# Kernel optimization log

Measured on AMD Instinct MI355X. Metric: run time of the kernel, lower is better.

Reference implementation:

```python
import jax, jax.numpy as jnp
import numpy as np

B, H, W, Z = 4, 256, 256, 64
ITERATIONS = 8
EPSILON = 1e-06
CENTER = 6.0  # 7-point Laplacian diagonal


def _stencil(x):
    # x: [B, H, W, Z]; zero (Dirichlet) boundaries via padded shifts
    west = jnp.pad(x[:, :, :-1, :], ((0, 0), (0, 0), (1, 0), (0, 0)))
    east = jnp.pad(x[:, :, 1:, :], ((0, 0), (0, 0), (0, 1), (0, 0)))
    north = jnp.pad(x[:, :-1, :, :], ((0, 0), (1, 0), (0, 0), (0, 0)))
    south = jnp.pad(x[:, 1:, :, :], ((0, 0), (0, 1), (0, 0), (0, 0)))
    bottom = jnp.pad(x[:, :, :, :-1], ((0, 0), (0, 0), (0, 0), (1, 0)))
    top = jnp.pad(x[:, :, :, 1:], ((0, 0), (0, 0), (0, 0), (0, 1)))
    return CENTER * x - west - east - south - north - bottom - top


def _dot(a, b):
    # per-sample dot product, keepdims for scalar broadcast
    return jnp.sum(a * b, axis=(1, 2, 3), keepdims=True)


def setup_inputs() -> dict:
    key = jax.random.key(0)
    k1, k2, k3 = jax.random.split(key, 3)
    shape = (B, H, W, Z)
    return {
        "x": jax.random.normal(k1, shape, dtype=jnp.float32),
        "b": jax.random.normal(k2, shape, dtype=jnp.float32),
        "reference_sol": jax.random.normal(k3, shape, dtype=jnp.float32),
    }


def reference(x, b, reference_sol):
    r = b - _stencil(x)
    p = r
    rho = _dot(r, r)

    def body(carry, _):
        x, r, p, rho = carry
        w = _stencil(p)
        eta = _dot(p, w)
        alpha = rho / (eta + EPSILON)
        x = x + alpha * p
        r = r - alpha * w
        rho_next = _dot(r, r)
        beta = rho_next / (rho + EPSILON)
        p = r + beta * p
        return (x, r, p, rho_next), None

    (x, r, p, rho), _ = jax.lax.scan(body, (x, r, p, rho), None, length=ITERATIONS)

    diff = x - reference_sol
    loss = jnp.mean(diff * diff)
    max_error = jnp.max(jnp.abs(diff))
    residual_norm_sq = jnp.mean(rho)
    return (loss, x, max_error, residual_norm_sq)
```

## Files before the change

### kernel.cpp

```cpp
#include <hip/hip_runtime.h>

#define B_ 4
#define H_ 256
#define W_ 256
#define Z_ 64
#define NB_ (H_*W_*Z_)
#define N_  (B_*NB_)
#define ITER_ 8
#define EPS_ 1e-6f
#define SLOTS_ 64

#define RHO_OFF   0
#define ETA_OFF   ((ITER_+1)*B_*SLOTS_)
#define LOSS_OFF  (ETA_OFF + ITER_*B_*SLOTS_)
#define MAXE_OFF  (LOSS_OFF + SLOTS_)
#define SCAL_FLOATS (MAXE_OFF + SLOTS_)

struct F8 { float4 a, b; };

__device__ __forceinline__ float wsum(float v){
  v += __shfl_xor(v,32); v += __shfl_xor(v,16); v += __shfl_xor(v,8);
  v += __shfl_xor(v,4);  v += __shfl_xor(v,2);  v += __shfl_xor(v,1);
  return v;
}
__device__ __forceinline__ float wmaxr(float v){
  v = fmaxf(v,__shfl_xor(v,32)); v = fmaxf(v,__shfl_xor(v,16));
  v = fmaxf(v,__shfl_xor(v,8));  v = fmaxf(v,__shfl_xor(v,4));
  v = fmaxf(v,__shfl_xor(v,2));  v = fmaxf(v,__shfl_xor(v,1));
  return v;
}
__device__ __forceinline__ float read_sum(const float* s){
  return wsum(s[threadIdx.x & 63]);
}
__device__ __forceinline__ void block_atomic_sum(float v, float* dst, float* lds){
  v = wsum(v);
  int wid = threadIdx.x >> 6, lane = threadIdx.x & 63;
  if (lane == 0) lds[wid] = v;
  __syncthreads();
  if (threadIdx.x == 0) atomicAdd(dst, lds[0]+lds[1]+lds[2]+lds[3]);
}

__device__ __forceinline__ float4 ld4(const float* p){ return *(const float4*)p; }

__device__ __forceinline__ void sten_core(const F8& c, const F8& wm, const F8& wp,
                                          const F8& hm, const F8& hp,
                                          float zl, float zr, F8& st)
{
  st.a.x = 6.f*c.a.x - wm.a.x - wp.a.x - hm.a.x - hp.a.x - zl     - c.a.y;
  st.a.y = 6.f*c.a.y - wm.a.y - wp.a.y - hm.a.y - hp.a.y - c.a.x  - c.a.z;
  st.a.z = 6.f*c.a.z - wm.a.z - wp.a.z - hm.a.z - hp.a.z - c.a.y  - c.a.w;
  st.a.w = 6.f*c.a.w - wm.a.w - wp.a.w - hm.a.w - hp.a.w - c.a.z  - c.b.x;
  st.b.x = 6.f*c.b.x - wm.b.x - wp.b.x - hm.b.x - hp.b.x - c.a.w  - c.b.y;
  st.b.y = 6.f*c.b.y - wm.b.y - wp.b.y - hm.b.y - hp.b.y - c.b.x  - c.b.z;
  st.b.z = 6.f*c.b.z - wm.b.z - wp.b.z - hm.b.z - hp.b.z - c.b.y  - c.b.w;
  st.b.w = 6.f*c.b.w - wm.b.w - wp.b.w - hm.b.w - hp.b.w - c.b.z  - zr;
}

__device__ __forceinline__ void stencil1(const float* __restrict__ a, int base,
                                         int w, int h, int zc, F8& c, F8& st)
{
  c.a = ld4(a+base); c.b = ld4(a+base+4);
  F8 zero; zero.a = make_float4(0,0,0,0); zero.b = zero.a;
  F8 wm = zero, wp = zero, hm = zero, hp = zero;
  if (w > 0)    { wm.a = ld4(a+base-Z_);    wm.b = ld4(a+base-Z_+4); }
  if (w < W_-1) { wp.a = ld4(a+base+Z_);    wp.b = ld4(a+base+Z_+4); }
  if (h > 0)    { hm.a = ld4(a+base-W_*Z_); hm.b = ld4(a+base-W_*Z_+4); }
  if (h < H_-1) { hp.a = ld4(a+base+W_*Z_); hp.b = ld4(a+base+W_*Z_+4); }
  float zl = (zc > 0) ? a[base-1] : 0.f;
  float zr = (zc < 7) ? a[base+8] : 0.f;
  sten_core(c, wm, wp, hm, hp, zl, zr, st);
}

__device__ __forceinline__ F8 comb8(const float* r, const float* p, float beta, int idx){
  F8 o;
  float4 ra = ld4(r+idx), rb = ld4(r+idx+4);
  float4 pa = ld4(p+idx), pb = ld4(p+idx+4);
  o.a.x = ra.x + beta*pa.x; o.a.y = ra.y + beta*pa.y;
  o.a.z = ra.z + beta*pa.z; o.a.w = ra.w + beta*pa.w;
  o.b.x = rb.x + beta*pb.x; o.b.y = rb.y + beta*pb.y;
  o.b.z = rb.z + beta*pb.z; o.b.w = rb.w + beta*pb.w;
  return o;
}
__device__ __forceinline__ void stencil2(const float* __restrict__ r,
                                         const float* __restrict__ p, float beta,
                                         int base, int w, int h, int zc,
                                         F8& c, F8& st)
{
  c = comb8(r,p,beta,base);
  F8 zero; zero.a = make_float4(0,0,0,0); zero.b = zero.a;
  F8 wm = zero, wp = zero, hm = zero, hp = zero;
  if (w > 0)    wm = comb8(r,p,beta,base-Z_);
  if (w < W_-1) wp = comb8(r,p,beta,base+Z_);
  if (h > 0)    hm = comb8(r,p,beta,base-W_*Z_);
  if (h < H_-1) hp = comb8(r,p,beta,base+W_*Z_);
  float zl = (zc > 0) ? r[base-1] + beta*p[base-1] : 0.f;
  float zr = (zc < 7) ? r[base+8] + beta*p[base+8] : 0.f;
  sten_core(c, wm, wp, hm, hp, zl, zr, st);
}

#define IDX_SETUP \
  const int zc = threadIdx.x & 7; \
  const int wl = threadIdx.x >> 3; \
  const int w  = blockIdx.x*32 + wl; \
  const int h  = blockIdx.y; \
  const int bb = blockIdx.z; \
  const int base = ((bb*H_ + h)*W_ + w)*Z_ + zc*8; \
  const int flat = (blockIdx.z*gridDim.y + blockIdx.y)*gridDim.x + blockIdx.x; \
  const int slot = flat & (SLOTS_-1);

__global__ __launch_bounds__(256) void k_init(const float* __restrict__ x,
                                              const float* __restrict__ b,
                                              float* __restrict__ r,
                                              float* scal)
{
  __shared__ float lds[4];
  IDX_SETUP
  F8 c, st;
  stencil1(x, base, w, h, zc, c, st);
  float4 b0 = ld4(b+base), b1 = ld4(b+base+4);
  F8 rv;
  rv.a = make_float4(b0.x-st.a.x, b0.y-st.a.y, b0.z-st.a.z, b0.w-st.a.w);
  rv.b = make_float4(b1.x-st.b.x, b1.y-st.b.y, b1.z-st.b.z, b1.w-st.b.w);
  *(float4*)(r+base)   = rv.a;
  *(float4*)(r+base+4) = rv.b;
  float rho = rv.a.x*rv.a.x + rv.a.y*rv.a.y + rv.a.z*rv.a.z + rv.a.w*rv.a.w
            + rv.b.x*rv.b.x + rv.b.y*rv.b.y + rv.b.z*rv.b.z + rv.b.w*rv.b.w;
  block_atomic_sum(rho, scal + RHO_OFF + (0*B_+bb)*SLOTS_ + slot, lds);
}

__global__ __launch_bounds__(256) void k_a0(const float* __restrict__ r,
                                            float* __restrict__ pnew,
                                            float* scal)
{
  __shared__ float lds[4];
  IDX_SETUP
  F8 c, st;
  stencil1(r, base, w, h, zc, c, st);
  *(float4*)(pnew+base)   = c.a;
  *(float4*)(pnew+base+4) = c.b;
  float eta = c.a.x*st.a.x + c.a.y*st.a.y + c.a.z*st.a.z + c.a.w*st.a.w
            + c.b.x*st.b.x + c.b.y*st.b.y + c.b.z*st.b.z + c.b.w*st.b.w;
  block_atomic_sum(eta, scal + ETA_OFF + (0*B_+bb)*SLOTS_ + slot, lds);
}

__global__ __launch_bounds__(256) void k_a(const float* __restrict__ r,
                                           const float* __restrict__ pold,
                                           float* __restrict__ pnew,
                                           float* scal, int it)
{
  __shared__ float lds[4];
  IDX_SETUP
  float num = read_sum(scal + RHO_OFF + (it*B_+bb)*SLOTS_);
  float den = read_sum(scal + RHO_OFF + ((it-1)*B_+bb)*SLOTS_);
  float beta = num / (den + EPS_);
  F8 c, st;
  stencil2(r, pold, beta, base, w, h, zc, c, st);
  *(float4*)(pnew+base)   = c.a;
  *(float4*)(pnew+base+4) = c.b;
  float eta = c.a.x*st.a.x + c.a.y*st.a.y + c.a.z*st.a.z + c.a.w*st.a.w
            + c.b.x*st.b.x + c.b.y*st.b.y + c.b.z*st.b.z + c.b.w*st.b.w;
  block_atomic_sum(eta, scal + ETA_OFF + (it*B_+bb)*SLOTS_ + slot, lds);
}

__global__ __launch_bounds__(256) void k_b(float* __restrict__ x,
                                           float* __restrict__ r,
                                           const float* __restrict__ p,
                                           float* scal, int it)
{
  __shared__ float lds[4];
  IDX_SETUP
  float num = read_sum(scal + RHO_OFF + (it*B_+bb)*SLOTS_);
  float den = read_sum(scal + ETA_OFF + (it*B_+bb)*SLOTS_);
  float alpha = num / (den + EPS_);
  F8 c, st;
  stencil1(p, base, w, h, zc, c, st);
  float4 x0 = ld4(x+base), x1 = ld4(x+base+4);
  x0.x += alpha*c.a.x; x0.y += alpha*c.a.y; x0.z += alpha*c.a.z; x0.w += alpha*c.a.w;
  x1.x += alpha*c.b.x; x1.y += alpha*c.b.y; x1.z += alpha*c.b.z; x1.w += alpha*c.b.w;
  *(float4*)(x+base)   = x0;
  *(float4*)(x+base+4) = x1;
  float4 r0 = ld4(r+base), r1 = ld4(r+base+4);
  r0.x -= alpha*st.a.x; r0.y -= alpha*st.a.y; r0.z -= alpha*st.a.z; r0.w -= alpha*st.a.w;
  r1.x -= alpha*st.b.x; r1.y -= alpha*st.b.y; r1.z -= alpha*st.b.z; r1.w -= alpha*st.b.w;
  *(float4*)(r+base)   = r0;
  *(float4*)(r+base+4) = r1;
  float rho = r0.x*r0.x + r0.y*r0.y + r0.z*r0.z + r0.w*r0.w
            + r1.x*r1.x + r1.y*r1.y + r1.z*r1.z + r1.w*r1.w;
  block_atomic_sum(rho, scal + RHO_OFF + ((it+1)*B_+bb)*SLOTS_ + slot, lds);
}

__global__ __launch_bounds__(256) void k_b_fin(const float* __restrict__ x,
                                               const float* __restrict__ r,
                                               const float* __restrict__ p,
                                               const float* __restrict__ ref,
                                               float* __restrict__ out,
                                               float* scal, int it)
{
  __shared__ float xs[2048];
  __shared__ float lds[12];
  IDX_SETUP
  float num = read_sum(scal + RHO_OFF + (it*B_+bb)*SLOTS_);
  float den = read_sum(scal + ETA_OFF + (it*B_+bb)*SLOTS_);
  float alpha = num / (den + EPS_);
  F8 c, st;
  stencil1(p, base, w, h, zc, c, st);
  float4 x0 = ld4(x+base), x1 = ld4(x+base+4);
  x0.x += alpha*c.a.x; x0.y += alpha*c.a.y; x0.z += alpha*c.a.z; x0.w += alpha*c.a.w;
  x1.x += alpha*c.b.x; x1.y += alpha*c.b.y; x1.z += alpha*c.b.z; x1.w += alpha*c.b.w;
  float4 r0 = ld4(r+base), r1 = ld4(r+base+4);
  r0.x -= alpha*st.a.x; r0.y -= alpha*st.a.y; r0.z -= alpha*st.a.z; r0.w -= alpha*st.a.w;
  r1.x -= alpha*st.b.x; r1.y -= alpha*st.b.y; r1.z -= alpha*st.b.z; r1.w -= alpha*st.b.w;
  float rho = r0.x*r0.x + r0.y*r0.y + r0.z*r0.z + r0.w*r0.w
            + r1.x*r1.x + r1.y*r1.y + r1.z*r1.z + r1.w*r1.w;

  const int t = threadIdx.x;
  xs[t*8+0] = x0.x; xs[t*8+1] = x0.y; xs[t*8+2] = x0.z; xs[t*8+3] = x0.w;
  xs[t*8+4] = x1.x; xs[t*8+5] = x1.y; xs[t*8+6] = x1.z; xs[t*8+7] = x1.w;

  float4 f0 = ld4(ref+base), f1 = ld4(ref+base+4);
  float d0 = x0.x-f0.x, d1 = x0.y-f0.y, d2 = x0.z-f0.z, d3 = x0.w-f0.w;
  float d4 = x1.x-f1.x, d5 = x1.y-f1.y, d6 = x1.z-f1.z, d7 = x1.w-f1.w;
  float loss = d0*d0+d1*d1+d2*d2+d3*d3+d4*d4+d5*d5+d6*d6+d7*d7;
  float me = fmaxf(fmaxf(fmaxf(fabsf(d0),fabsf(d1)),fmaxf(fabsf(d2),fabsf(d3))),
                   fmaxf(fmaxf(fabsf(d4),fabsf(d5)),fmaxf(fabsf(d6),fabsf(d7))));

  float rs = wsum(rho), ls = wsum(loss), ms = wmaxr(me);
  int wid = t >> 6, lane = t & 63;
  if (lane == 0) { lds[wid] = rs; lds[4+wid] = ls; lds[8+wid] = ms; }
  __syncthreads();
  if (t == 0) {
    atomicAdd(scal + RHO_OFF + ((it+1)*B_+bb)*SLOTS_ + slot, lds[0]+lds[1]+lds[2]+lds[3]);
    atomicAdd(scal + LOSS_OFF + slot, lds[4]+lds[5]+lds[6]+lds[7]);
    float bm = fmaxf(fmaxf(lds[8],lds[9]), fmaxf(lds[10],lds[11]));
    atomicMax((unsigned int*)(scal + MAXE_OFF) + slot, __float_as_uint(bm));
  }

  const int S = flat * 2048;
  #pragma unroll
  for (int c2 = 0; c2 < 2; ++c2) {
    int q = t + 256*c2;
    if (q < 511) {
      float4 v = make_float4(xs[3+4*q], xs[4+4*q], xs[5+4*q], xs[6+4*q]);
      *(float4*)(out + S + 4 + 4*q) = v;
    } else if (q == 511) {
      out[S+1] = xs[0]; out[S+2] = xs[1]; out[S+3] = xs[2];
      out[S+2048] = xs[2047];
    }
  }
}

__global__ __launch_bounds__(64) void k_scal(const float* scal, float* out)
{
  int lane = threadIdx.x;
  float loss = wsum(scal[LOSS_OFF + lane]);
  float me   = wmaxr(__uint_as_float(((const unsigned int*)scal)[MAXE_OFF + lane]));
  float rho_sum = 0.f;
  for (int bb = 0; bb < B_; ++bb)
    rho_sum += wsum(scal[RHO_OFF + (ITER_*B_+bb)*SLOTS_ + lane]);
  if (lane == 0) {
    out[0]      = loss / (float)N_;
    out[1+N_]   = me;
    out[2+N_]   = rho_sum / (float)B_;
  }
}

extern "C" void kernel_launch(void* const* d_in, const int* in_sizes, int n_in,
                              void* d_out, int out_size, void* d_ws, size_t ws_size,
                              hipStream_t stream) {
  float* x         = (float*)d_in[0];
  const float* b   = (const float*)d_in[1];
  const float* ref = (const float*)d_in[2];
  float* out       = (float*)d_out;

  float* r  = (float*)d_ws;
  float* p0 = r + N_;
  float* p1;
  float* scal;
  size_t need3 = ((size_t)3*N_ + SCAL_FLOATS) * sizeof(float);
  if (ws_size >= need3) {
    p1   = p0 + N_;
    scal = p1 + N_;
  } else {
    p1   = (float*)d_out;
    scal = p0 + N_;
  }

  (void)hipMemsetAsync(scal, 0, SCAL_FLOATS*sizeof(float), stream);

  dim3 grid(W_/32, H_, B_), blk(256);
  k_init<<<grid, blk, 0, stream>>>(x, b, r, scal);

  float* pa = p1;
  float* pb = p0;
  for (int it = 0; it < ITER_; ++it) {
    if (it == 0)
      k_a0<<<grid, blk, 0, stream>>>(r, pa, scal);
    else
      k_a<<<grid, blk, 0, stream>>>(r, pb, pa, scal, it);
    if (it < ITER_-1)
      k_b<<<grid, blk, 0, stream>>>(x, r, pa, scal, it);
    else
      k_b_fin<<<grid, blk, 0, stream>>>(x, r, pa, ref, out, scal, it);
    float* t = pa; pa = pb; pb = t;
  }

  k_scal<<<1, 64, 0, stream>>>(scal, out);
}
```

Measured before the change: 1.097 ms.

## Fuse all CG phases into one persistent kernel with a software grid barrier

Replaces the 17 separate kernel launches with a single persistent kernel of 2048 blocks. Each block walks four tiles per phase, and the phases are separated by a hand-written atomic grid barrier built from 64 counters plus a generation flag. It also fetches the z-neighbour halo with wavefront shuffles instead of extra global loads, and pads the LDS staging buffer used in the final x write. This is meant to remove launch gaps and kernel tail effects, but it depends on all 2048 blocks being resident at once (launch bounds 256x8) or the barrier deadlocks, and each barrier adds spin-wait latency.

New measurement: 3.344 ms. +204.8%, slower.

```diff
diff --git a/kernel.cpp b/kernel.cpp
--- a/kernel.cpp
+++ b/kernel.cpp
@@ -10,11 +10,19 @@
 #define EPS_ 1e-6f
 #define SLOTS_ 64
 
+#define GRID_  2048
+#define TPB_   256
+#define NTILE_ 8192
+#define TILES_ (NTILE_/GRID_)
+static_assert(NTILE_ % GRID_ == 0, "tile split");
+
 #define RHO_OFF   0
 #define ETA_OFF   ((ITER_+1)*B_*SLOTS_)
 #define LOSS_OFF  (ETA_OFF + ITER_*B_*SLOTS_)
 #define MAXE_OFF  (LOSS_OFF + SLOTS_)
-#define SCAL_FLOATS (MAXE_OFF + SLOTS_)
+#define BAR_OFF   (MAXE_OFF + SLOTS_)
+#define GEN_OFF   (BAR_OFF + 64)
+#define SCAL_FLOATS (GEN_OFF + 32)
 
 struct F8 { float4 a, b; };
 
@@ -38,37 +46,42 @@
   if (lane == 0) lds[wid] = v;
   __syncthreads();
   if (threadIdx.x == 0) atomicAdd(dst, lds[0]+lds[1]+lds[2]+lds[3]);
+  __syncthreads();
 }
 
 __device__ __forceinline__ float4 ld4(const float* p){ return *(const float4*)p; }
 
-__device__ __forceinline__ void sten_core(const F8& c, const F8& wm, const F8& wp,
-                                          const F8& hm, const F8& hp,
-                                          float zl, float zr, F8& st)
-{
-  st.a.x = 6.f*c.a.x - wm.a.x - wp.a.x - hm.a.x - hp.a.x - zl     - c.a.y;
-  st.a.y = 6.f*c.a.y - wm.a.y - wp.a.y - hm.a.y - hp.a.y - c.a.x  - c.a.z;
-  st.a.z = 6.f*c.a.z - wm.a.z - wp.a.z - hm.a.z - hp.a.z - c.a.y  - c.a.w;
-  st.a.w = 6.f*c.a.w - wm.a.w - wp.a.w - hm.a.w - hp.a.w - c.a.z  - c.b.x;
-  st.b.x = 6.f*c.b.x - wm.b.x - wp.b.x - hm.b.x - hp.b.x - c.a.w  - c.b.y;
-  st.b.y = 6.f*c.b.y - wm.b.y - wp.b.y - hm.b.y - hp.b.y - c.b.x  - c.b.z;
-  st.b.z = 6.f*c.b.z - wm.b.z - wp.b.z - hm.b.z - hp.b.z - c.b.y  - c.b.w;
-  st.b.w = 6.f*c.b.w - wm.b.w - wp.b.w - hm.b.w - hp.b.w - c.b.z  - zr;
+__device__ __forceinline__ void sub8(F8& s, const F8& n){
+  s.a.x-=n.a.x; s.a.y-=n.a.y; s.a.z-=n.a.z; s.a.w-=n.a.w;
+  s.b.x-=n.b.x; s.b.y-=n.b.y; s.b.z-=n.b.z; s.b.w-=n.b.w;
+}
+
+__device__ __forceinline__ void zcore(const F8& c, int zc, F8& st){
+  const int lane = threadIdx.x & 63;
+  float zl = __shfl(c.b.w, (lane-1)&63);
+  float zr = __shfl(c.a.x, (lane+1)&63);
+  zl = (zc > 0) ? zl : 0.f;
+  zr = (zc < 7) ? zr : 0.f;
+  st.a.x = 6.f*c.a.x - zl    - c.a.y;
+  st.a.y = 6.f*c.a.y - c.a.x - c.a.z;
+  st.a.z = 6.f*c.a.z - c.a.y - c.a.w;
+  st.a.w = 6.f*c.a.w - c.a.z - c.b.x;
+  st.b.x = 6.f*c.b.x - c.a.w - c.b.y;
+  st.b.y = 6.f*c.b.y - c.b.x - c.b.z;
+  st.b.z = 6.f*c.b.z - c.b.y - c.b.w;
+  st.b.w = 6.f*c.b.w - c.b.z - zr;
 }
 
 __device__ __forceinline__ void stencil1(const float* __restrict__ a, int base,
                                          int w, int h, int zc, F8& c, F8& st)
 {
   c.a = ld4(a+base); c.b = ld4(a+base+4);
-  F8 zero; zero.a = make_float4(0,0,0,0); zero.b = zero.a;
-  F8 wm = zero, wp = zero, hm = zero, hp = zero;
-  if (w > 0)    { wm.a = ld4(a+base-Z_);    wm.b = ld4(a+base-Z_+4); }
-  if (w < W_-1) { wp.a = ld4(a+base+Z_);    wp.b = ld4(a+base+Z_+4); }
-  if (h > 0)    { hm.a = ld4(a+base-W_*Z_); hm.b = ld4(a+base-W_*Z_+4); }
-  if (h < H_-1) { hp.a = ld4(a+base+W_*Z_); hp.b = ld4(a+base+W_*Z_+4); }
-  float zl = (zc > 0) ? a[base-1] : 0.f;
-  float zr = (zc < 7) ? a[base+8] : 0.f;
-  sten_core(c, wm, wp, hm, hp, zl, zr, st);
+  zcore(c, zc, st);
+  F8 t;
+  if (w > 0)    { t.a = ld4(a+base-Z_);    t.b = ld4(a+base-Z_+4);    sub8(st,t); }
+  if (w < W_-1) { t.a = ld4(a+base+Z_);    t.b = ld4(a+base+Z_+4);    sub8(st,t); }
+  if (h > 0)    { t.a = ld4(a+base-W_*Z_); t.b = ld4(a+base-W_*Z_+4); sub8(st,t); }
+  if (h < H_-1) { t.a = ld4(a+base+W_*Z_); t.b = ld4(a+base+W_*Z_+4); sub8(st,t); }
 }
 
 __device__ __forceinline__ F8 comb8(const float* r, const float* p, float beta, int idx){
@@ -87,180 +100,220 @@
                                          F8& c, F8& st)
 {
   c = comb8(r,p,beta,base);
-  F8 zero; zero.a = make_float4(0,0,0,0); zero.b = zero.a;
-  F8 wm = zero, wp = zero, hm = zero, hp = zero;
-  if (w > 0)    wm = comb8(r,p,beta,base-Z_);
-  if (w < W_-1) wp = comb8(r,p,beta,base+Z_);
-  if (h > 0)    hm = comb8(r,p,beta,base-W_*Z_);
-  if (h < H_-1) hp = comb8(r,p,beta,base+W_*Z_);
-  float zl = (zc > 0) ? r[base-1] + beta*p[base-1] : 0.f;
-  float zr = (zc < 7) ? r[base+8] + beta*p[base+8] : 0.f;
-  sten_core(c, wm, wp, hm, hp, zl, zr, st);
-}
-
-#define IDX_SETUP \
-  const int zc = threadIdx.x & 7; \
-  const int wl = threadIdx.x >> 3; \
-  const int w  = blockIdx.x*32 + wl; \
-  const int h  = blockIdx.y; \
-  const int bb = blockIdx.z; \
-  const int base = ((bb*H_ + h)*W_ + w)*Z_ + zc*8; \
-  const int flat = (blockIdx.z*gridDim.y + blockIdx.y)*gridDim.x + blockIdx.x; \
-  const int slot = flat & (SLOTS_-1);
-
-__global__ __launch_bounds__(256) void k_init(const float* __restrict__ x,
-                                              const float* __restrict__ b,
-                                              float* __restrict__ r,
-                                              float* scal)
+  zcore(c, zc, st);
+  if (w > 0)    sub8(st, comb8(r,p,beta,base-Z_));
+  if (w < W_-1) sub8(st, comb8(r,p,beta,base+Z_));
+  if (h > 0)    sub8(st, comb8(r,p,beta,base-W_*Z_));
+  if (h < H_-1) sub8(st, comb8(r,p,beta,base+W_*Z_));
+}
+
+__device__ __forceinline__ void gsync(unsigned* bars, unsigned* gen, unsigned epoch){
+  __syncthreads();
+  if (threadIdx.x == 0) {
+    __threadfence();
+    __hip_atomic_fetch_add(&bars[blockIdx.x & 63], 1u,
+                           __ATOMIC_RELAXED, __HIP_MEMORY_SCOPE_AGENT);
+  }
+  if (blockIdx.x == 0) {
+    if (threadIdx.x < 64) {
+      const unsigned tgt = epoch * (GRID_/64);
+      while (__hip_atomic_load(&bars[threadIdx.x],
+                               __ATOMIC_RELAXED, __HIP_MEMORY_SCOPE_AGENT) < tgt)
+        __builtin_amdgcn_s_sleep(2);
+    }
+    __syncthreads();
+    if (threadIdx.x == 0) {
+      __threadfence();
+      __hip_atomic_fetch_add(gen, 1u, __ATOMIC_RELAXED, __HIP_MEMORY_SCOPE_AGENT);
+    }
+  } else {
+    if (threadIdx.x == 0) {
+      while (__hip_atomic_load(gen, __ATOMIC_RELAXED,
+                               __HIP_MEMORY_SCOPE_AGENT) < epoch)
+        __builtin_amdgcn_s_sleep(2);
+      __threadfence();
+    }
+  }
+  __syncthreads();
+}
+
+#define TILE_OF(j) ((((int)(blockIdx.x >> 3) * TILES_ + (j)) << 3) | (int)(blockIdx.x & 7))
+
+#define TILE_SETUP(T) \
+  const int tx = (T) & 7; \
+  const int hh = ((T) >> 3) & 255; \
+  const int bb = (T) >> 11; \
+  const int w  = tx*32 + wl; \
+  const int base = ((bb*H_ + hh)*W_ + w)*Z_ + zc*8; \
+  const int slot = (T) & 63;
+
+#define XI(k) ((((k) >> 3)*9) + ((k) & 7))
+
+__global__ __launch_bounds__(TPB_, 8)
+void k_cg(float* x, const float* __restrict__ bv, const float* __restrict__ ref,
+          float* out, float* __restrict__ r, float* p0, float* p1,
+          float* __restrict__ scal)
 {
-  __shared__ float lds[4];
-  IDX_SETUP
-  F8 c, st;
-  stencil1(x, base, w, h, zc, c, st);
-  float4 b0 = ld4(b+base), b1 = ld4(b+base+4);
-  F8 rv;
-  rv.a = make_float4(b0.x-st.a.x, b0.y-st.a.y, b0.z-st.a.z, b0.w-st.a.w);
-  rv.b = make_float4(b1.x-st.b.x, b1.y-st.b.y, b1.z-st.b.z, b1.w-st.b.w);
-  *(float4*)(r+base)   = rv.a;
-  *(float4*)(r+base+4) = rv.b;
-  float rho = rv.a.x*rv.a.x + rv.a.y*rv.a.y + rv.a.z*rv.a.z + rv.a.w*rv.a.w
-            + rv.b.x*rv.b.x + rv.b.y*rv.b.y + rv.b.z*rv.b.z + rv.b.w*rv.b.w;
-  block_atomic_sum(rho, scal + RHO_OFF + (0*B_+bb)*SLOTS_ + slot, lds);
-}
-
-__global__ __launch_bounds__(256) void k_a0(const float* __restrict__ r,
-                                            float* __restrict__ pnew,
-                                            float* scal)
-{
-  __shared__ float lds[4];
-  IDX_SETUP
-  F8 c, st;
-  stencil1(r, base, w, h, zc, c, st);
-  *(float4*)(pnew+base)   = c.a;
-  *(float4*)(pnew+base+4) = c.b;
-  float eta = c.a.x*st.a.x + c.a.y*st.a.y + c.a.z*st.a.z + c.a.w*st.a.w
-            + c.b.x*st.b.x + c.b.y*st.b.y + c.b.z*st.b.z + c.b.w*st.b.w;
-  block_atomic_sum(eta, scal + ETA_OFF + (0*B_+bb)*SLOTS_ + slot, lds);
-}
-
-__global__ __launch_bounds__(256) void k_a(const float* __restrict__ r,
-                                           const float* __restrict__ pold,
-                                           float* __restrict__ pnew,
-                                           float* scal, int it)
-{
-  __shared__ float lds[4];
-  IDX_SETUP
-  float num = read_sum(scal + RHO_OFF + (it*B_+bb)*SLOTS_);
-  float den = read_sum(scal + RHO_OFF + ((it-1)*B_+bb)*SLOTS_);
-  float beta = num / (den + EPS_);
-  F8 c, st;
-  stencil2(r, pold, beta, base, w, h, zc, c, st);
-  *(float4*)(pnew+base)   = c.a;
-  *(float4*)(pnew+base+4) = c.b;
-  float eta = c.a.x*st.a.x + c.a.y*st.a.y + c.a.z*st.a.z + c.a.w*st.a.w
-            + c.b.x*st.b.x + c.b.y*st.b.y + c.b.z*st.b.z + c.b.w*st.b.w;
-  block_atomic_sum(eta, scal + ETA_OFF + (it*B_+bb)*SLOTS_ + slot, lds);
-}
-
-__global__ __launch_bounds__(256) void k_b(float* __restrict__ x,
-                                           float* __restrict__ r,
-                                           const float* __restrict__ p,
-                                           float* scal, int it)
-{
-  __shared__ float lds[4];
-  IDX_SETUP
-  float num = read_sum(scal + RHO_OFF + (it*B_+bb)*SLOTS_);
-  float den = read_sum(scal + ETA_OFF + (it*B_+bb)*SLOTS_);
-  float alpha = num / (den + EPS_);
-  F8 c, st;
-  stencil1(p, base, w, h, zc, c, st);
-  float4 x0 = ld4(x+base), x1 = ld4(x+base+4);
-  x0.x += alpha*c.a.x; x0.y += alpha*c.a.y; x0.z += alpha*c.a.z; x0.w += alpha*c.a.w;
-  x1.x += alpha*c.b.x; x1.y += alpha*c.b.y; x1.z += alpha*c.b.z; x1.w += alpha*c.b.w;
-  *(float4*)(x+base)   = x0;
-  *(float4*)(x+base+4) = x1;
-  float4 r0 = ld4(r+base), r1 = ld4(r+base+4);
-  r0.x -= alpha*st.a.x; r0.y -= alpha*st.a.y; r0.z -= alpha*st.a.z; r0.w -= alpha*st.a.w;
-  r1.x -= alpha*st.b.x; r1.y -= alpha*st.b.y; r1.z -= alpha*st.b.z; r1.w -= alpha*st.b.w;
-  *(float4*)(r+base)   = r0;
-  *(float4*)(r+base+4) = r1;
-  float rho = r0.x*r0.x + r0.y*r0.y + r0.z*r0.z + r0.w*r0.w
-            + r1.x*r1.x + r1.y*r1.y + r1.z*r1.z + r1.w*r1.w;
-  block_atomic_sum(rho, scal + RHO_OFF + ((it+1)*B_+bb)*SLOTS_ + slot, lds);
-}
-
-__global__ __launch_bounds__(256) void k_b_fin(const float* __restrict__ x,
-                                               const float* __restrict__ r,
-                                               const float* __restrict__ p,
-                                               const float* __restrict__ ref,
-                                               float* __restrict__ out,
-                                               float* scal, int it)
-{
-  __shared__ float xs[2048];
+  __shared__ float xs[256*9];
   __shared__ float lds[12];
-  IDX_SETUP
-  float num = read_sum(scal + RHO_OFF + (it*B_+bb)*SLOTS_);
-  float den = read_sum(scal + ETA_OFF + (it*B_+bb)*SLOTS_);
-  float alpha = num / (den + EPS_);
-  F8 c, st;
-  stencil1(p, base, w, h, zc, c, st);
-  float4 x0 = ld4(x+base), x1 = ld4(x+base+4);
-  x0.x += alpha*c.a.x; x0.y += alpha*c.a.y; x0.z += alpha*c.a.z; x0.w += alpha*c.a.w;
-  x1.x += alpha*c.b.x; x1.y += alpha*c.b.y; x1.z += alpha*c.b.z; x1.w += alpha*c.b.w;
-  float4 r0 = ld4(r+base), r1 = ld4(r+base+4);
-  r0.x -= alpha*st.a.x; r0.y -= alpha*st.a.y; r0.z -= alpha*st.a.z; r0.w -= alpha*st.a.w;
-  r1.x -= alpha*st.b.x; r1.y -= alpha*st.b.y; r1.z -= alpha*st.b.z; r1.w -= alpha*st.b.w;
-  float rho = r0.x*r0.x + r0.y*r0.y + r0.z*r0.z + r0.w*r0.w
-            + r1.x*r1.x + r1.y*r1.y + r1.z*r1.z + r1.w*r1.w;
-
-  const int t = threadIdx.x;
-  xs[t*8+0] = x0.x; xs[t*8+1] = x0.y; xs[t*8+2] = x0.z; xs[t*8+3] = x0.w;
-  xs[t*8+4] = x1.x; xs[t*8+5] = x1.y; xs[t*8+6] = x1.z; xs[t*8+7] = x1.w;
-
-  float4 f0 = ld4(ref+base), f1 = ld4(ref+base+4);
-  float d0 = x0.x-f0.x, d1 = x0.y-f0.y, d2 = x0.z-f0.z, d3 = x0.w-f0.w;
-  float d4 = x1.x-f1.x, d5 = x1.y-f1.y, d6 = x1.z-f1.z, d7 = x1.w-f1.w;
-  float loss = d0*d0+d1*d1+d2*d2+d3*d3+d4*d4+d5*d5+d6*d6+d7*d7;
-  float me = fmaxf(fmaxf(fmaxf(fabsf(d0),fabsf(d1)),fmaxf(fabsf(d2),fabsf(d3))),
-                   fmaxf(fmaxf(fabsf(d4),fabsf(d5)),fmaxf(fabsf(d6),fabsf(d7))));
-
-  float rs = wsum(rho), ls = wsum(loss), ms = wmaxr(me);
-  int wid = t >> 6, lane = t & 63;
-  if (lane == 0) { lds[wid] = rs; lds[4+wid] = ls; lds[8+wid] = ms; }
-  __syncthreads();
-  if (t == 0) {
-    atomicAdd(scal + RHO_OFF + ((it+1)*B_+bb)*SLOTS_ + slot, lds[0]+lds[1]+lds[2]+lds[3]);
-    atomicAdd(scal + LOSS_OFF + slot, lds[4]+lds[5]+lds[6]+lds[7]);
-    float bm = fmaxf(fmaxf(lds[8],lds[9]), fmaxf(lds[10],lds[11]));
-    atomicMax((unsigned int*)(scal + MAXE_OFF) + slot, __float_as_uint(bm));
-  }
-
-  const int S = flat * 2048;
-  #pragma unroll
-  for (int c2 = 0; c2 < 2; ++c2) {
-    int q = t + 256*c2;
-    if (q < 511) {
-      float4 v = make_float4(xs[3+4*q], xs[4+4*q], xs[5+4*q], xs[6+4*q]);
-      *(float4*)(out + S + 4 + 4*q) = v;
-    } else if (q == 511) {
-      out[S+1] = xs[0]; out[S+2] = xs[1]; out[S+3] = xs[2];
-      out[S+2048] = xs[2047];
-    }
-  }
-}
-
-__global__ __launch_bounds__(64) void k_scal(const float* scal, float* out)
-{
-  int lane = threadIdx.x;
-  float loss = wsum(scal[LOSS_OFF + lane]);
-  float me   = wmaxr(__uint_as_float(((const unsigned int*)scal)[MAXE_OFF + lane]));
-  float rho_sum = 0.f;
-  for (int bb = 0; bb < B_; ++bb)
-    rho_sum += wsum(scal[RHO_OFF + (ITER_*B_+bb)*SLOTS_ + lane]);
-  if (lane == 0) {
-    out[0]      = loss / (float)N_;
-    out[1+N_]   = me;
-    out[2+N_]   = rho_sum / (float)B_;
+  unsigned* bars = (unsigned*)(scal + BAR_OFF);
+  unsigned* gen  = (unsigned*)(scal + GEN_OFF);
+
+  const int zc = threadIdx.x & 7;
+  const int wl = threadIdx.x >> 3;
+  const int t  = threadIdx.x;
+  unsigned ep = 0;
+
+  #pragma unroll 1
+  for (int j = 0; j < TILES_; ++j) {
+    const int T = TILE_OF(j);
+    TILE_SETUP(T)
+    F8 c, st;
+    stencil1(x, base, w, hh, zc, c, st);
+    float4 b0 = ld4(bv+base), b1 = ld4(bv+base+4);
+    F8 rv;
+    rv.a = make_float4(b0.x-st.a.x, b0.y-st.a.y, b0.z-st.a.z, b0.w-st.a.w);
+    rv.b = make_float4(b1.x-st.b.x, b1.y-st.b.y, b1.z-st.b.z, b1.w-st.b.w);
+    *(float4*)(r+base)   = rv.a;
+    *(float4*)(r+base+4) = rv.b;
+    float rho = rv.a.x*rv.a.x + rv.a.y*rv.a.y + rv.a.z*rv.a.z + rv.a.w*rv.a.w
+              + rv.b.x*rv.b.x + rv.b.y*rv.b.y + rv.b.z*rv.b.z + rv.b.w*rv.b.w;
+    block_atomic_sum(rho, scal + RHO_OFF + (0*B_+bb)*SLOTS_ + slot, lds);
+  }
+  gsync(bars, gen, ++ep);
+
+  float* pa = p1;
+  float* pb = p0;
+
+  for (int it = 0; it < ITER_; ++it) {
+    if (it == 0) {
+      #pragma unroll 1
+      for (int j = 0; j < TILES_; ++j) {
+        const int T = TILE_OF(j);
+        TILE_SETUP(T)
+        F8 c, st;
+        stencil1(r, base, w, hh, zc, c, st);
+        *(float4*)(pa+base)   = c.a;
+        *(float4*)(pa+base+4) = c.b;
+        float eta = c.a.x*st.a.x + c.a.y*st.a.y + c.a.z*st.a.z + c.a.w*st.a.w
+                  + c.b.x*st.b.x + c.b.y*st.b.y + c.b.z*st.b.z + c.b.w*st.b.w;
+        block_atomic_sum(eta, scal + ETA_OFF + (0*B_+bb)*SLOTS_ + slot, lds);
+      }
+    } else {
+      #pragma unroll 1
+      for (int j = 0; j < TILES_; ++j) {
+        const int T = TILE_OF(j);
+        TILE_SETUP(T)
+        float num = read_sum(scal + RHO_OFF + (it*B_+bb)*SLOTS_);
+        float den = read_sum(scal + RHO_OFF + ((it-1)*B_+bb)*SLOTS_);
+        float beta = num / (den + EPS_);
+        F8 c, st;
+        stencil2(r, pb, beta, base, w, hh, zc, c, st);
+        *(float4*)(pa+base)   = c.a;
+        *(float4*)(pa+base+4) = c.b;
+        float eta = c.a.x*st.a.x + c.a.y*st.a.y + c.a.z*st.a.z + c.a.w*st.a.w
+                  + c.b.x*st.b.x + c.b.y*st.b.y + c.b.z*st.b.z + c.b.w*st.b.w;
+        block_atomic_sum(eta, scal + ETA_OFF + (it*B_+bb)*SLOTS_ + slot, lds);
+      }
+    }
+    gsync(bars, gen, ++ep);
+
+    if (it < ITER_-1) {
+      #pragma unroll 1
+      for (int j = 0; j < TILES_; ++j) {
+        const int T = TILE_OF(j);
+        TILE_SETUP(T)
+        float num = read_sum(scal + RHO_OFF + (it*B_+bb)*SLOTS_);
+        float den = read_sum(scal + ETA_OFF + (it*B_+bb)*SLOTS_);
+        float alpha = num / (den + EPS_);
+        F8 c, st;
+        stencil1(pa, base, w, hh, zc, c, st);
+        float4 x0 = ld4(x+base), x1 = ld4(x+base+4);
+        x0.x += alpha*c.a.x; x0.y += alpha*c.a.y; x0.z += alpha*c.a.z; x0.w += alpha*c.a.w;
+        x1.x += alpha*c.b.x; x1.y += alpha*c.b.y; x1.z += alpha*c.b.z; x1.w += alpha*c.b.w;
+        *(float4*)(x+base)   = x0;
+        *(float4*)(x+base+4) = x1;
+        float4 r0 = ld4(r+base), r1 = ld4(r+base+4);
+        r0.x -= alpha*st.a.x; r0.y -= alpha*st.a.y; r0.z -= alpha*st.a.z; r0.w -= alpha*st.a.w;
+        r1.x -= alpha*st.b.x; r1.y -= alpha*st.b.y; r1.z -= alpha*st.b.z; r1.w -= alpha*st.b.w;
+        *(float4*)(r+base)   = r0;
+        *(float4*)(r+base+4) = r1;
+        float rho = r0.x*r0.x + r0.y*r0.y + r0.z*r0.z + r0.w*r0.w
+                  + r1.x*r1.x + r1.y*r1.y + r1.z*r1.z + r1.w*r1.w;
+        block_atomic_sum(rho, scal + RHO_OFF + ((it+1)*B_+bb)*SLOTS_ + slot, lds);
+      }
+    } else {
+      #pragma unroll 1
+      for (int j = 0; j < TILES_; ++j) {
+        const int T = TILE_OF(j);
+        TILE_SETUP(T)
+        float num = read_sum(scal + RHO_OFF + (it*B_+bb)*SLOTS_);
+        float den = read_sum(scal + ETA_OFF + (it*B_+bb)*SLOTS_);
+        float alpha = num / (den + EPS_);
+        F8 c, st;
+        stencil1(pa, base, w, hh, zc, c, st);
+        float4 x0 = ld4(x+base), x1 = ld4(x+base+4);
+        x0.x += alpha*c.a.x; x0.y += alpha*c.a.y; x0.z += alpha*c.a.z; x0.w += alpha*c.a.w;
+        x1.x += alpha*c.b.x; x1.y += alpha*c.b.y; x1.z += alpha*c.b.z; x1.w += alpha*c.b.w;
+        float4 r0 = ld4(r+base), r1 = ld4(r+base+4);
+        r0.x -= alpha*st.a.x; r0.y -= alpha*st.a.y; r0.z -= alpha*st.a.z; r0.w -= alpha*st.a.w;
+        r1.x -= alpha*st.b.x; r1.y -= alpha*st.b.y; r1.z -= alpha*st.b.z; r1.w -= alpha*st.b.w;
+        float rho = r0.x*r0.x + r0.y*r0.y + r0.z*r0.z + r0.w*r0.w
+                  + r1.x*r1.x + r1.y*r1.y + r1.z*r1.z + r1.w*r1.w;
+
+        xs[t*9+0] = x0.x; xs[t*9+1] = x0.y; xs[t*9+2] = x0.z; xs[t*9+3] = x0.w;
+        xs[t*9+4] = x1.x; xs[t*9+5] = x1.y; xs[t*9+6] = x1.z; xs[t*9+7] = x1.w;
+
+        float4 f0 = ld4(ref+base), f1 = ld4(ref+base+4);
+        float d0 = x0.x-f0.x, d1 = x0.y-f0.y, d2 = x0.z-f0.z, d3 = x0.w-f0.w;
+        float d4 = x1.x-f1.x, d5 = x1.y-f1.y, d6 = x1.z-f1.z, d7 = x1.w-f1.w;
+        float loss = d0*d0+d1*d1+d2*d2+d3*d3+d4*d4+d5*d5+d6*d6+d7*d7;
+        float me = fmaxf(fmaxf(fmaxf(fabsf(d0),fabsf(d1)),fmaxf(fabsf(d2),fabsf(d3))),
+                         fmaxf(fmaxf(fabsf(d4),fabsf(d5)),fmaxf(fabsf(d6),fabsf(d7))));
+
+        float rs = wsum(rho), ls = wsum(loss), ms = wmaxr(me);
+        int wid = t >> 6, lane = t & 63;
+        if (lane == 0) { lds[wid] = rs; lds[4+wid] = ls; lds[8+wid] = ms; }
+        __syncthreads();
+        if (t == 0) {
+          atomicAdd(scal + RHO_OFF + ((it+1)*B_+bb)*SLOTS_ + slot, lds[0]+lds[1]+lds[2]+lds[3]);
+          atomicAdd(scal + LOSS_OFF + slot, lds[4]+lds[5]+lds[6]+lds[7]);
+          float bm = fmaxf(fmaxf(lds[8],lds[9]), fmaxf(lds[10],lds[11]));
+          atomicMax((unsigned int*)(scal + MAXE_OFF) + slot, __float_as_uint(bm));
+        }
+
+        const int S = T * 2048;
+        #pragma unroll
+        for (int c2 = 0; c2 < 2; ++c2) {
+          int q = t + 256*c2;
+          if (q < 511) {
+            int k = 4*q + 3;
+            float4 v = make_float4(xs[XI(k)], xs[XI(k+1)], xs[XI(k+2)], xs[XI(k+3)]);
+            *(float4*)(out + S + 4 + 4*q) = v;
+          } else if (q == 511) {
+            out[S+1] = xs[XI(0)]; out[S+2] = xs[XI(1)]; out[S+3] = xs[XI(2)];
+            out[S+2048] = xs[XI(2047)];
+          }
+        }
+        __syncthreads();
+      }
+    }
+    gsync(bars, gen, ++ep);
+    float* tmp = pa; pa = pb; pb = tmp;
+  }
+
+  if (blockIdx.x == 0 && t < 64) {
+    int lane = t;
+    float loss = wsum(scal[LOSS_OFF + lane]);
+    float me   = wmaxr(__uint_as_float(((const unsigned int*)scal)[MAXE_OFF + lane]));
+    float rho_sum = 0.f;
+    for (int bb = 0; bb < B_; ++bb)
+      rho_sum += wsum(scal[RHO_OFF + (ITER_*B_+bb)*SLOTS_ + lane]);
+    if (lane == 0) {
+      out[0]    = loss / (float)N_;
+      out[1+N_] = me;
+      out[2+N_] = rho_sum / (float)B_;
+    }
   }
 }
 
@@ -268,7 +321,7 @@
                               void* d_out, int out_size, void* d_ws, size_t ws_size,
                               hipStream_t stream) {
   float* x         = (float*)d_in[0];
-  const float* b   = (const float*)d_in[1];
+  const float* bv  = (const float*)d_in[1];
   const float* ref = (const float*)d_in[2];
   float* out       = (float*)d_out;
 
@@ -281,28 +334,11 @@
     p1   = p0 + N_;
     scal = p1 + N_;
   } else {
-    p1   = (float*)d_out;
+    p1   = out;
     scal = p0 + N_;
   }
 
   (void)hipMemsetAsync(scal, 0, SCAL_FLOATS*sizeof(float), stream);
 
-  dim3 grid(W_/32, H_, B_), blk(256);
-  k_init<<<grid, blk, 0, stream>>>(x, b, r, scal);
-
-  float* pa = p1;
-  float* pb = p0;
-  for (int it = 0; it < ITER_; ++it) {
-    if (it == 0)
-      k_a0<<<grid, blk, 0, stream>>>(r, pa, scal);
-    else
-      k_a<<<grid, blk, 0, stream>>>(r, pb, pa, scal, it);
-    if (it < ITER_-1)
-      k_b<<<grid, blk, 0, stream>>>(x, r, pa, scal, it);
-    else
-      k_b_fin<<<grid, blk, 0, stream>>>(x, r, pa, ref, out, scal, it);
-    float* t = pa; pa = pb; pb = t;
-  }
-
-  k_scal<<<1, 64, 0, stream>>>(scal, out);
-}
+  k_cg<<<dim3(GRID_), dim3(TPB_), 0, stream>>>(x, bv, ref, out, r, p0, p1, scal);
+}
```
